# Performance work log

Measured on AMD Instinct MI355X. Metric: run time of the kernel, lower is better.

Reference implementation:

```python
import jax, jax.numpy as jnp
import numpy as np

EPS = 1e-3  # keras LayerNormalization default epsilon


def layer_norm(x, gamma, beta):
    mean = jnp.mean(x, axis=-1, keepdims=True)
    var = jnp.var(x, axis=-1, keepdims=True)
    return (x - mean) * jax.lax.rsqrt(var + EPS) * gamma + beta


def setup_inputs() -> dict:
    key = jax.random.key(0)
    ks = jax.random.split(key, 8)
    B, H, W, C = 16, 64, 64, 512
    IC = C // 8  # intermediate_channel = 64
    x = jax.random.normal(ks[0], (B, H, W, C), dtype=jnp.float32)
    s = 1.0 / np.sqrt(C)
    w_f = jax.random.normal(ks[1], (C, IC), dtype=jnp.float32) * s
    w_h = jax.random.normal(ks[2], (C, IC), dtype=jnp.float32) * s
    w_fgh = jax.random.normal(ks[3], (IC, C), dtype=jnp.float32) / np.sqrt(IC)
    gamma_f = jnp.ones((IC,), jnp.float32)
    beta_f = jnp.zeros((IC,), jnp.float32)
    gamma_h = jnp.ones((IC,), jnp.float32)
    beta_h = jnp.zeros((IC,), jnp.float32)
    gamma_fgh = jnp.ones((C,), jnp.float32)
    beta_fgh = jnp.zeros((C,), jnp.float32)
    scale = jnp.ones((1,), jnp.float32)  # non-negative scalar gate
    return {"x": x, "w_f": w_f, "w_h": w_h, "w_fgh": w_fgh,
            "gamma_f": gamma_f, "beta_f": beta_f,
            "gamma_h": gamma_h, "beta_h": beta_h,
            "gamma_fgh": gamma_fgh, "beta_fgh": beta_fgh,
            "scale": scale}


def reference(x, w_f, w_h, w_fgh, gamma_f, beta_f, gamma_h, beta_h,
              gamma_fgh, beta_fgh, scale):
    # NOTE: faithful to the source, which (re)uses w_f/LN_f for BOTH f and g,
    # and combines f and g with an ELEMENTWISE multiply (not a matmul).
    g = layer_norm(jnp.einsum("bhwc,ci->bhwi", x, w_f), gamma_f, beta_f)  # (B,H,W,IC)
    f = jnp.transpose(g, (0, 2, 1, 3))  # Permute(2,1,3): (B,W,H,IC)
    h = layer_norm(jnp.einsum("bhwc,ci->bhwi", x, w_h), gamma_h, beta_h)
    a = jax.nn.softmax(f * g, axis=1)  # softmax over axis 1 (H==W required)
    y = jnp.einsum("bhwi,ic->bhwc", a * h, w_fgh)
    y = layer_norm(y, gamma_fgh, beta_fgh) * scale  # scalar gate
    return x + y  # residual add
```

## Files before the change

### kernel.cpp

```cpp
#include <hip/hip_runtime.h>

#define EPSN 1e-3f

typedef __attribute__((ext_vector_type(8))) short short8;
typedef __attribute__((ext_vector_type(4))) float floatx4;

__device__ __forceinline__ unsigned f2bf_pack(float a, float b) {
    unsigned ua = __builtin_bit_cast(unsigned, a);
    ua += 0x7FFF + ((ua >> 16) & 1);
    unsigned ub = __builtin_bit_cast(unsigned, b);
    ub += 0x7FFF + ((ub >> 16) & 1);
    return (ua >> 16) | (ub & 0xFFFF0000u);
}
__device__ __forceinline__ unsigned short f2bf(float f) {
    unsigned u = __builtin_bit_cast(unsigned, f);
    u += 0x7FFF + ((u >> 16) & 1);
    return (unsigned short)(u >> 16);
}
__device__ __forceinline__ float bf2f(unsigned short u) {
    unsigned v = ((unsigned)u) << 16;
    return __builtin_bit_cast(float, v);
}

__device__ __forceinline__ void gload_lds16(const unsigned short* g, unsigned short* l) {
    __builtin_amdgcn_global_load_lds(
        (const __attribute__((address_space(1))) unsigned int*)g,
        (__attribute__((address_space(3))) unsigned int*)l,
        16, 0, 0);
}

__global__ void k0_convert(const float* __restrict__ w_f,
                           const float* __restrict__ w_h,
                           const float* __restrict__ w_fgh,
                           unsigned short* __restrict__ Wgh,
                           unsigned short* __restrict__ Wf3)
{
    int tid = blockIdx.x * 256 + threadIdx.x;
    if (tid < 8192) {
        int n16 = tid & 15, k8 = (tid >> 4) & 63, ntile = tid >> 10;
        int n = ntile * 16 + n16;
        const float* src = (n < 64) ? (w_f + n) : (w_h + (n - 64));
        unsigned short o[8];
        #pragma unroll
        for (int j = 0; j < 8; ++j) o[j] = f2bf(src[(size_t)(k8 * 8 + j) * 64]);
        *(uint4*)&Wgh[(size_t)tid * 8] = *(const uint4*)o;
    } else if (tid < 12288) {
        int id = tid - 8192;
        int n16 = id & 15, k8 = (id >> 4) & 7, ntile = id >> 7;
        int n = ntile * 16 + n16;
        unsigned short o[8];
        #pragma unroll
        for (int j = 0; j < 8; ++j) o[j] = f2bf(w_fgh[(size_t)(k8 * 8 + j) * 512 + n]);
        *(uint4*)&Wf3[(size_t)id * 8] = *(const uint4*)o;
    }
}

__global__ __launch_bounds__(256, 4) void k1_gemm_ln(
    const float* __restrict__ x,
    const unsigned short* __restrict__ Wgh,
    const float* __restrict__ gamma_f, const float* __restrict__ beta_f,
    const float* __restrict__ gamma_h, const float* __restrict__ beta_h,
    float* __restrict__ g_out, unsigned short* __restrict__ h_out)
{
    __shared__ unsigned short Blds[2][8192];

    const int t = threadIdx.x;
    const int lane = t & 63;
    const int wv = t >> 6;
    const int quad = lane >> 4;
    const int n16 = lane & 15;
    const int row_base = blockIdx.x * 64 + wv * 16;

    floatx4 acc[8];
    #pragma unroll
    for (int ct = 0; ct < 8; ++ct) acc[ct] = (floatx4){0.f, 0.f, 0.f, 0.f};

    const float* xrow = x + (size_t)(row_base + n16) * 512 + quad * 8;
    const unsigned short* bsrc = Wgh + (size_t)lane * 8;

    auto stage = [&](int par, int ch) {
        #pragma unroll
        for (int i = 0; i < 4; ++i) {
            int s = wv * 4 + i;
            int cl = s >> 3, ct = s & 7;
            gload_lds16(bsrc + (size_t)ct * 8192 + (ch * 2 + cl) * 512,
                        &Blds[par][s * 512]);
        }
    };

    stage(0, 0);
    float4 u[2], v[2];
    u[0] = *(const float4*)(xrow);
    v[0] = *(const float4*)(xrow + 4);
    u[1] = *(const float4*)(xrow + 32);
    v[1] = *(const float4*)(xrow + 36);
    __syncthreads();

    #pragma unroll
    for (int ch = 0; ch < 8; ++ch) {
        const int par = ch & 1;
        if (ch < 7) stage(par ^ 1, ch + 1);
        float4 un[2], vn[2];
        if (ch < 7) {
            un[0] = *(const float4*)(xrow + ch * 64 + 64);
            vn[0] = *(const float4*)(xrow + ch * 64 + 68);
            un[1] = *(const float4*)(xrow + ch * 64 + 96);
            vn[1] = *(const float4*)(xrow + ch * 64 + 100);
        }
        #pragma unroll
        for (int cl = 0; cl < 2; ++cl) {
            union { short8 s; uint4 q; } cvt;
            cvt.q = make_uint4(f2bf_pack(u[cl].x, u[cl].y), f2bf_pack(u[cl].z, u[cl].w),
                               f2bf_pack(v[cl].x, v[cl].y), f2bf_pack(v[cl].z, v[cl].w));
            short8 a = cvt.s;
            #pragma unroll
            for (int ct = 0; ct < 8; ++ct) {
                short8 b = *(const short8*)&Blds[par][(cl * 8 + ct) * 512 + lane * 8];
                acc[ct] = __builtin_amdgcn_mfma_f32_16x16x32_bf16(a, b, acc[ct], 0, 0, 0);
            }
        }
        if (ch < 7) {
            u[0] = un[0]; v[0] = vn[0]; u[1] = un[1]; v[1] = vn[1];
        }
        __syncthreads();
    }

    #pragma unroll
    for (int half = 0; half < 2; ++half) {
        float s[4] = {0.f, 0.f, 0.f, 0.f}, s2[4] = {0.f, 0.f, 0.f, 0.f};
        #pragma unroll
        for (int c0 = 0; c0 < 4; ++c0) {
            int ct = half * 4 + c0;
            #pragma unroll
            for (int r = 0; r < 4; ++r) {
                float val = acc[ct][r];
                s[r] += val; s2[r] += val * val;
            }
        }
        #pragma unroll
        for (int off = 1; off <= 8; off <<= 1)
            #pragma unroll
            for (int r = 0; r < 4; ++r) {
                s[r]  += __shfl_xor(s[r],  off, 64);
                s2[r] += __shfl_xor(s2[r], off, 64);
            }
        float mean[4], rstd[4];
        #pragma unroll
        for (int r = 0; r < 4; ++r) {
            mean[r] = s[r] * (1.f / 64.f);
            float var = s2[r] * (1.f / 64.f) - mean[r] * mean[r];
            rstd[r] = rsqrtf(var + EPSN);
        }
        #pragma unroll
        for (int c0 = 0; c0 < 4; ++c0) {
            int ct = half * 4 + c0;
            int col = c0 * 16 + n16;
            float gm = half ? gamma_h[col] : gamma_f[col];
            float bt = half ? beta_h[col]  : beta_f[col];
            #pragma unroll
            for (int r = 0; r < 4; ++r) {
                int row = row_base + quad * 4 + r;
                float val = (acc[ct][r] - mean[r]) * rstd[r] * gm + bt;
                if (half == 0)
                    g_out[(size_t)row * 64 + col] = val;
                else
                    h_out[(size_t)row * 64 + col] = f2bf(val);
            }
        }
    }
}

__global__ __launch_bounds__(256, 6) void k2_softmax(
    const float* __restrict__ g_in,
    const unsigned short* __restrict__ h_in,
    unsigned short* __restrict__ t_out)
{
    __shared__ float S[64 * 64];
    __shared__ float pmax[4 * 64];
    __shared__ float psum[4 * 64];
    __shared__ float colmax[64];
    __shared__ float colinv[64];

    const int t = threadIdx.x;
    const int b = blockIdx.x >> 6;
    const int w = blockIdx.x & 63;
    const size_t base1 = (size_t)(b * 64 + w) * 4096;

    #pragma unroll
    for (int p = 0; p < 4; ++p) {
        int hh = p * 16 + (t >> 4);
        int ii0 = (t & 15) * 4;
        float4 gf = *(const float4*)&g_in[base1 + hh * 64 + ii0];
        float4 gg = *(const float4*)&g_in[(size_t)((b * 64 + hh) * 64 + w) * 64 + ii0];
        float4 sv;
        sv.x = gf.x * gg.x; sv.y = gf.y * gg.y;
        sv.z = gf.z * gg.z; sv.w = gf.w * gg.w;
        *(float4*)&S[hh * 64 + ii0] = sv;
    }
    __syncthreads();

    const int q = t >> 6;
    const int i = t & 63;
    float m = -1e30f;
    #pragma unroll
    for (int r = 0; r < 16; ++r)
        m = fmaxf(m, S[(q * 16 + r) * 64 + i]);
    pmax[q * 64 + i] = m;
    __syncthreads();
    if (t < 64)
        colmax[i] = fmaxf(fmaxf(pmax[i], pmax[64 + i]),
                          fmaxf(pmax[128 + i], pmax[192 + i]));
    __syncthreads();
    const float cm = colmax[i];
    float s = 0.f;
    #pragma unroll
    for (int r = 0; r < 16; ++r) {
        int idx = (q * 16 + r) * 64 + i;
        float e = __expf(S[idx] - cm);
        S[idx] = e;
        s += e;
    }
    psum[q * 64 + i] = s;
    __syncthreads();
    if (t < 64)
        colinv[i] = 1.f / (psum[i] + psum[64 + i] + psum[128 + i] + psum[192 + i]);
    __syncthreads();

    {
        const int hh = t >> 2;
        const int ii0 = (t & 3) * 16;
        const size_t rowg = (size_t)((b * 64 + hh) * 64 + w) * 64;
        float4 sv[4], ci[4];
        ushort4 hv[4];
        #pragma unroll
        for (int k = 0; k < 4; ++k) {
            sv[k] = *(const float4*)&S[hh * 64 + ii0 + k * 4];
            ci[k] = *(const float4*)&colinv[ii0 + k * 4];
            hv[k] = *(const ushort4*)&h_in[rowg + ii0 + k * 4];
        }
        uint4 o0, o1;
        o0.x = f2bf_pack(sv[0].x * ci[0].x * bf2f(hv[0].x), sv[0].y * ci[0].y * bf2f(hv[0].y));
        o0.y = f2bf_pack(sv[0].z * ci[0].z * bf2f(hv[0].z), sv[0].w * ci[0].w * bf2f(hv[0].w));
        o0.z = f2bf_pack(sv[1].x * ci[1].x * bf2f(hv[1].x), sv[1].y * ci[1].y * bf2f(hv[1].y));
        o0.w = f2bf_pack(sv[1].z * ci[1].z * bf2f(hv[1].z), sv[1].w * ci[1].w * bf2f(hv[1].w));
        o1.x = f2bf_pack(sv[2].x * ci[2].x * bf2f(hv[2].x), sv[2].y * ci[2].y * bf2f(hv[2].y));
        o1.y = f2bf_pack(sv[2].z * ci[2].z * bf2f(hv[2].z), sv[2].w * ci[2].w * bf2f(hv[2].w));
        o1.z = f2bf_pack(sv[3].x * ci[3].x * bf2f(hv[3].x), sv[3].y * ci[3].y * bf2f(hv[3].y));
        o1.w = f2bf_pack(sv[3].z * ci[3].z * bf2f(hv[3].z), sv[3].w * ci[3].w * bf2f(hv[3].w));
        *(uint4*)&t_out[rowg + ii0] = o0;
        *(uint4*)&t_out[rowg + ii0 + 8] = o1;
    }
}

__global__ __launch_bounds__(256, 4) void k3_gemm_ln_res(
    const unsigned short* __restrict__ tmat,
    const unsigned short* __restrict__ Wf3,
    const float* __restrict__ gamma, const float* __restrict__ beta,
    const float* __restrict__ scale,
    const float* __restrict__ x,
    float* __restrict__ out)
{
    __shared__ float bounce[4][16 * 132];
    __shared__ float2 exch[4][16];

    const int t = threadIdx.x;
    const int lane = t & 63;
    const int wv = t >> 6;
    const int quad = lane >> 4;
    const int n16 = lane & 15;
    const int rowtile = blockIdx.x * 2 + (wv >> 1);
    const int half = wv & 1;

    const unsigned short* trow = tmat + (size_t)(rowtile * 16 + n16) * 64 + quad * 8;
    short8 a0 = *(const short8*)trow;
    short8 a1 = *(const short8*)(trow + 32);

    floatx4 acc[16];
    #pragma unroll
    for (int nt = 0; nt < 16; ++nt) acc[nt] = (floatx4){0.f, 0.f, 0.f, 0.f};
    #pragma unroll
    for (int nt = 0; nt < 16; ++nt) {
        int ngt = half * 16 + nt;
        short8 b0 = *(const short8*)&Wf3[(size_t)((ngt * 8 + quad) * 16 + n16) * 8];
        short8 b1 = *(const short8*)&Wf3[(size_t)((ngt * 8 + 4 + quad) * 16 + n16) * 8];
        acc[nt] = __builtin_amdgcn_mfma_f32_16x16x32_bf16(a0, b0, acc[nt], 0, 0, 0);
        acc[nt] = __builtin_amdgcn_mfma_f32_16x16x32_bf16(a1, b1, acc[nt], 0, 0, 0);
    }

    float s[4] = {0.f, 0.f, 0.f, 0.f}, s2[4] = {0.f, 0.f, 0.f, 0.f};
    #pragma unroll
    for (int nt = 0; nt < 16; ++nt)
        #pragma unroll
        for (int r = 0; r < 4; ++r) {
            float v = acc[nt][r];
            s[r] += v; s2[r] += v * v;
        }
    #pragma unroll
    for (int off = 1; off <= 8; off <<= 1)
        #pragma unroll
        for (int r = 0; r < 4; ++r) {
            s[r]  += __shfl_xor(s[r],  off, 64);
            s2[r] += __shfl_xor(s2[r], off, 64);
        }
    if (n16 == 0) {
        #pragma unroll
        for (int r = 0; r < 4; ++r)
            exch[wv][quad * 4 + r] = make_float2(s[r], s2[r]);
    }
    __syncthreads();
    float mean[4], rstd[4];
    #pragma unroll
    for (int r = 0; r < 4; ++r) {
        float2 o = exch[wv ^ 1][quad * 4 + r];
        float st = s[r] + o.x, st2 = s2[r] + o.y;
        mean[r] = st * (1.f / 512.f);
        float var = st2 * (1.f / 512.f) - mean[r] * mean[r];
        rstd[r] = rsqrtf(var + EPSN);
    }
    const float sc = scale[0];

    #pragma unroll
    for (int chunk = 0; chunk < 2; ++chunk) {
        __syncthreads();
        #pragma unroll
        for (int n0 = 0; n0 < 8; ++n0) {
            int nt = chunk * 8 + n0;
            int col = half * 256 + nt * 16 + n16;
            float gm = gamma[col], bt = beta[col];
            #pragma unroll
            for (int r = 0; r < 4; ++r)
                bounce[wv][(quad * 4 + r) * 132 + n0 * 16 + n16] =
                    sc * ((acc[nt][r] - mean[r]) * rstd[r] * gm + bt);
        }
        __syncthreads();
        #pragma unroll
        for (int pass = 0; pass < 8; ++pass) {
            int row = pass * 2 + (lane >> 5);
            int coff = (lane & 31) * 4;
            float4 v = *(const float4*)&bounce[wv][row * 132 + coff];
            size_t gidx = ((size_t)rowtile * 16 + row) * 512 + half * 256 + chunk * 128 + coff;
            float4 xv = *(const float4*)&x[gidx];
            float4 o;
            o.x = xv.x + v.x; o.y = xv.y + v.y; o.z = xv.z + v.z; o.w = xv.w + v.w;
            *(float4*)&out[gidx] = o;
        }
    }
}

extern "C" void kernel_launch(void* const* d_in, const int* in_sizes, int n_in,
                              void* d_out, int out_size, void* d_ws, size_t ws_size,
                              hipStream_t stream) {
    const float* x         = (const float*)d_in[0];
    const float* w_f       = (const float*)d_in[1];
    const float* w_h       = (const float*)d_in[2];
    const float* w_fgh     = (const float*)d_in[3];
    const float* gamma_f   = (const float*)d_in[4];
    const float* beta_f    = (const float*)d_in[5];
    const float* gamma_h   = (const float*)d_in[6];
    const float* beta_h    = (const float*)d_in[7];
    const float* gamma_fgh = (const float*)d_in[8];
    const float* beta_fgh  = (const float*)d_in[9];
    const float* scale     = (const float*)d_in[10];
    float* out = (float*)d_out;

    char* wsb = (char*)d_ws;
    float* g            = (float*)wsb;
    unsigned short* h   = (unsigned short*)(wsb + 16777216);
    unsigned short* tm  = (unsigned short*)(wsb + 25165824);
    unsigned short* Wgh = (unsigned short*)(wsb + 33554432);
    unsigned short* Wf3 = (unsigned short*)(wsb + 33685504);

    k0_convert<<<48, 256, 0, stream>>>(w_f, w_h, w_fgh, Wgh, Wf3);
    k1_gemm_ln<<<1024, 256, 0, stream>>>(x, Wgh, gamma_f, beta_f,
                                         gamma_h, beta_h, g, h);
    k2_softmax<<<1024, 256, 0, stream>>>(g, h, tm);
    k3_gemm_ln_res<<<2048, 256, 0, stream>>>(tm, Wf3, gamma_fgh, beta_fgh,
                                             scale, x, out);
}
```

Before: 294.7 us.

## Stage x tiles through LDS with async global-to-LDS loads in GEMM

The first GEMM kernel now loads x rows into a swizzled LDS buffer with global_load_lds instead of per-lane register float4 loads. It shrinks the K chunk from 64 to 32, giving 16 iterations with double buffering for both the weight and x tiles. The goal is fully coalesced, asynchronous x loads that overlap with MFMA work and fewer live registers. The cost is twice as many barriers and extra LDS reads for the A operand.

```diff
diff --git a/kernel.cpp b/kernel.cpp
--- a/kernel.cpp
+++ b/kernel.cpp
@@ -23,6 +23,12 @@
 }
 
 __device__ __forceinline__ void gload_lds16(const unsigned short* g, unsigned short* l) {
+    __builtin_amdgcn_global_load_lds(
+        (const __attribute__((address_space(1))) unsigned int*)g,
+        (__attribute__((address_space(3))) unsigned int*)l,
+        16, 0, 0);
+}
+__device__ __forceinline__ void gload_lds16f(const float* g, float* l) {
     __builtin_amdgcn_global_load_lds(
         (const __attribute__((address_space(1))) unsigned int*)g,
         (__attribute__((address_space(3))) unsigned int*)l,
@@ -62,65 +68,63 @@
     const float* __restrict__ gamma_h, const float* __restrict__ beta_h,
     float* __restrict__ g_out, unsigned short* __restrict__ h_out)
 {
-    __shared__ unsigned short Blds[2][8192];
+    __shared__ unsigned short Blds[2][4096];
+    __shared__ float Xlds[2][2048];
 
     const int t = threadIdx.x;
     const int lane = t & 63;
     const int wv = t >> 6;
     const int quad = lane >> 4;
     const int n16 = lane & 15;
-    const int row_base = blockIdx.x * 64 + wv * 16;
+    const int row_base0 = blockIdx.x * 64;
+    const int row_base = row_base0 + wv * 16;
 
     floatx4 acc[8];
     #pragma unroll
     for (int ct = 0; ct < 8; ++ct) acc[ct] = (floatx4){0.f, 0.f, 0.f, 0.f};
 
-    const float* xrow = x + (size_t)(row_base + n16) * 512 + quad * 8;
-    const unsigned short* bsrc = Wgh + (size_t)lane * 8;
-
-    auto stage = [&](int par, int ch) {
-        #pragma unroll
-        for (int i = 0; i < 4; ++i) {
-            int s = wv * 4 + i;
-            int cl = s >> 3, ct = s & 7;
-            gload_lds16(bsrc + (size_t)ct * 8192 + (ch * 2 + cl) * 512,
-                        &Blds[par][s * 512]);
+    auto stageB = [&](int par, int c) {
+        #pragma unroll
+        for (int i = 0; i < 2; ++i) {
+            int ct = wv * 2 + i;
+            gload_lds16(Wgh + (size_t)(ct * 64 + c * 4) * 128 + lane * 8,
+                        &Blds[par][ct * 512]);
         }
     };
-
-    stage(0, 0);
-    float4 u[2], v[2];
-    u[0] = *(const float4*)(xrow);
-    v[0] = *(const float4*)(xrow + 4);
-    u[1] = *(const float4*)(xrow + 32);
-    v[1] = *(const float4*)(xrow + 36);
-    __syncthreads();
-
-    #pragma unroll
-    for (int ch = 0; ch < 8; ++ch) {
-        const int par = ch & 1;
-        if (ch < 7) stage(par ^ 1, ch + 1);
-        float4 un[2], vn[2];
-        if (ch < 7) {
-            un[0] = *(const float4*)(xrow + ch * 64 + 64);
-            vn[0] = *(const float4*)(xrow + ch * 64 + 68);
-            un[1] = *(const float4*)(xrow + ch * 64 + 96);
-            vn[1] = *(const float4*)(xrow + ch * 64 + 100);
-        }
-        #pragma unroll
-        for (int cl = 0; cl < 2; ++cl) {
-            union { short8 s; uint4 q; } cvt;
-            cvt.q = make_uint4(f2bf_pack(u[cl].x, u[cl].y), f2bf_pack(u[cl].z, u[cl].w),
-                               f2bf_pack(v[cl].x, v[cl].y), f2bf_pack(v[cl].z, v[cl].w));
-            short8 a = cvt.s;
-            #pragma unroll
-            for (int ct = 0; ct < 8; ++ct) {
-                short8 b = *(const short8*)&Blds[par][(cl * 8 + ct) * 512 + lane * 8];
-                acc[ct] = __builtin_amdgcn_mfma_f32_16x16x32_bf16(a, b, acc[ct], 0, 0, 0);
-            }
-        }
-        if (ch < 7) {
-            u[0] = un[0]; v[0] = vn[0]; u[1] = un[1]; v[1] = vn[1];
+    auto stageX = [&](int par, int c) {
+        #pragma unroll
+        for (int i = 0; i < 2; ++i) {
+            int ins = wv * 2 + i;
+            int rsub = lane >> 3;
+            int cb = ((lane & 7) * 16) ^ (rsub << 4);
+            gload_lds16f(x + (size_t)(row_base0 + ins * 8 + rsub) * 512
+                           + c * 32 + (cb >> 2),
+                         &Xlds[par][ins * 256]);
+        }
+    };
+
+    stageB(0, 0);
+    stageX(0, 0);
+    __syncthreads();
+
+    const int rl = wv * 16 + n16;
+    const int swz = (n16 & 7) << 4;
+
+    for (int c = 0; c < 16; ++c) {
+        const int par = c & 1;
+        if (c < 15) { stageB(par ^ 1, c + 1); stageX(par ^ 1, c + 1); }
+
+        const char* xr = (const char*)&Xlds[par][rl * 32];
+        float4 u = *(const float4*)(xr + ((quad * 32) ^ swz));
+        float4 v = *(const float4*)(xr + ((quad * 32 + 16) ^ swz));
+        union { short8 s; uint4 q; } cvt;
+        cvt.q = make_uint4(f2bf_pack(u.x, u.y), f2bf_pack(u.z, u.w),
+                           f2bf_pack(v.x, v.y), f2bf_pack(v.z, v.w));
+        short8 a = cvt.s;
+        #pragma unroll
+        for (int ct = 0; ct < 8; ++ct) {
+            short8 b = *(const short8*)&Blds[par][ct * 512 + lane * 8];
+            acc[ct] = __builtin_amdgcn_mfma_f32_16x16x32_bf16(a, b, acc[ct], 0, 0, 0);
         }
         __syncthreads();
     }
```

Measured after the change: 297.9 us. About the same (+1.1%).
